# Performance work log

Hardware: AMD Instinct MI355X
Metric: run time of the kernel (lower is better)

Reference implementation:

```python
import jax, jax.numpy as jnp
import numpy as np

N = 10000
E = 160000
IN_CH = 128
HID = 128
HEADS = 4
OUT_CH = 1  # forced by nn.Linear(heads, 1) applied after conv2


def _linear_params(key, out_f, in_f):
    k1, k2 = jax.random.split(key)
    bound = 1.0 / np.sqrt(in_f)
    W = jax.random.uniform(k1, (out_f, in_f), jnp.float32, -bound, bound)
    b = jax.random.uniform(k2, (out_f,), jnp.float32, -bound, bound)
    return W, b


def setup_inputs() -> dict:
    key = jax.random.key(0)
    ks = jax.random.split(key, 12)
    x = jax.random.normal(ks[0], (N, IN_CH), jnp.float32)
    edge_index = jax.random.randint(ks[1], (2, E), 0, N, jnp.int64)

    # conv1: TransformerConv(IN_CH, HID, HEADS)
    Wq1, bq1 = _linear_params(ks[2], HEADS * HID, IN_CH)
    Wk1, bk1 = _linear_params(ks[3], HEADS * HID, IN_CH)
    Wv1, bv1 = _linear_params(ks[4], HEADS * HID, IN_CH)
    Ws1, bs1 = _linear_params(ks[5], HEADS * HID, IN_CH)  # root/skip

    # conv2: TransformerConv(HID*HEADS, OUT_CH, HEADS)
    d2 = HID * HEADS
    Wq2, bq2 = _linear_params(ks[6], HEADS * OUT_CH, d2)
    Wk2, bk2 = _linear_params(ks[7], HEADS * OUT_CH, d2)
    Wv2, bv2 = _linear_params(ks[8], HEADS * OUT_CH, d2)
    Ws2, bs2 = _linear_params(ks[9], HEADS * OUT_CH, d2)

    # final nn.Linear(HEADS, 1)
    Wl, bl = _linear_params(ks[10], 1, HEADS)

    return dict(x=x, edge_index=edge_index,
                Wq1=Wq1, bq1=bq1, Wk1=Wk1, bk1=bk1, Wv1=Wv1, bv1=bv1, Ws1=Ws1, bs1=bs1,
                Wq2=Wq2, bq2=bq2, Wk2=Wk2, bk2=bk2, Wv2=Wv2, bv2=bv2, Ws2=Ws2, bs2=bs2,
                Wl=Wl, bl=bl)


def transformer_conv(x, edge_index, Wq, bq, Wk, bk, Wv, bv, Ws, bs, heads, ch):
    # PyG TransformerConv defaults: concat=True, root_weight=True, beta=False
    n = x.shape[0]
    q = (x @ Wq.T + bq).reshape(n, heads, ch)
    k = (x @ Wk.T + bk).reshape(n, heads, ch)
    v = (x @ Wv.T + bv).reshape(n, heads, ch)

    src, dst = edge_index[0], edge_index[1]  # messages flow src -> dst
    # per-edge attention logits [E, H]
    logits = jnp.einsum('ehc,ehc->eh', q[dst], k[src]) / np.sqrt(ch).astype(np.float32)

    # segment softmax over edges grouped by destination node
    seg_max = jax.ops.segment_max(logits, dst, num_segments=n)  # [N, H]
    seg_max = jnp.where(jnp.isfinite(seg_max), seg_max, 0.0)
    ex = jnp.exp(logits - seg_max[dst])
    denom = jax.ops.segment_sum(ex, dst, num_segments=n)  # [N, H]
    alpha = ex / jnp.maximum(denom[dst], 1e-16)  # [E, H]

    # scatter-aggregate weighted values
    msgs = alpha[:, :, None] * v[src]  # [E, H, C]
    out = jax.ops.segment_sum(msgs, dst, num_segments=n)  # [N, H, C]
    out = out.reshape(n, heads * ch)
    # root/skip connection
    return out + (x @ Ws.T + bs)


def reference(x, edge_index,
              Wq1, bq1, Wk1, bk1, Wv1, bv1, Ws1, bs1,
              Wq2, bq2, Wk2, bk2, Wv2, bv2, Ws2, bs2,
              Wl, bl):
    h = transformer_conv(x, edge_index, Wq1, bq1, Wk1, bk1, Wv1, bv1, Ws1, bs1, HEADS, HID)
    h = jax.nn.relu(h)
    # dropout is identity in eval mode
    h = transformer_conv(h, edge_index, Wq2, bq2, Wk2, bk2, Wv2, bv2, Ws2, bs2, HEADS, OUT_CH)
    h = h @ Wl.T + bl  # [N, 1]
    return jnp.mean(h, axis=0, keepdims=True)  # [1, 1]
```

## Files before the change

kernel.cpp:

```cpp
#include <hip/hip_runtime.h>
#include <math.h>

#define NN 10000
#define NE 160000
#define NROWT 79
#define NGEMM (NROWT * 32)

typedef __attribute__((ext_vector_type(8))) short bf16x8;
typedef __attribute__((ext_vector_type(4))) float f32x4;
typedef __attribute__((ext_vector_type(2))) float f32x2;

#if defined(__has_builtin)
#if __has_builtin(__builtin_amdgcn_cvt_pk_fp8_f32) && __has_builtin(__builtin_amdgcn_cvt_pk_f32_fp8)
#define HW_FP8 1
#endif
#endif

__device__ inline ushort f2bf(float x) {
  uint u = __float_as_uint(x);
  return (ushort)((u + 0x7fffu + ((u >> 16) & 1u)) >> 16);
}

__device__ inline void unpack8(uint4 u, float* f) {
  f[0] = __uint_as_float(u.x << 16); f[1] = __uint_as_float(u.x & 0xffff0000u);
  f[2] = __uint_as_float(u.y << 16); f[3] = __uint_as_float(u.y & 0xffff0000u);
  f[4] = __uint_as_float(u.z << 16); f[5] = __uint_as_float(u.z & 0xffff0000u);
  f[6] = __uint_as_float(u.w << 16); f[7] = __uint_as_float(u.w & 0xffff0000u);
}

#ifndef HW_FP8
__device__ inline float fp8_dec1(uint b) {
  uint s = b >> 7, e = (b >> 3) & 15, m = b & 7;
  float v = (e == 0) ? ldexpf((float)m, -9) : ldexpf((float)(8 + m), (int)e - 10);
  return s ? -v : v;
}
__device__ inline uint fp8_enc1(float x) {
  uint s = (__float_as_uint(x) >> 31) << 7;
  float a = fabsf(x);
  if (!(a < 448.f)) return s | 0x7e;
  if (a < 9.765625e-4f) return s;
  int e; float m = frexpf(a, &e);
  int E = e - 1, q;
  if (E < -6) {
    q = (int)rintf(ldexpf(a, 9));
    if (q == 0) return s;
    if (q >= 8) return s | 8;
    return s | (uint)q;
  }
  q = (int)rintf(ldexpf(m, 4));
  if (q == 16) { q = 8; ++E; }
  if (E > 8 || (E == 8 && q == 15)) return s | 0x7e;
  return s | ((uint)(E + 7) << 3) | (uint)(q - 8);
}
#endif

__device__ inline uint pack4_fp8(float a, float b, float c, float d) {
#ifdef HW_FP8
  uint w = (uint)__builtin_amdgcn_cvt_pk_fp8_f32(a, b, 0, false);
  w = (uint)__builtin_amdgcn_cvt_pk_fp8_f32(c, d, (int)w, true);
  return w;
#else
  return fp8_enc1(a) | (fp8_enc1(b) << 8) | (fp8_enc1(c) << 16) | (fp8_enc1(d) << 24);
#endif
}

__device__ inline void dec8_fp8(uint lo, uint hi, float* f) {
#ifdef HW_FP8
  f32x2 p0 = __builtin_amdgcn_cvt_pk_f32_fp8((int)lo, false);
  f32x2 p1 = __builtin_amdgcn_cvt_pk_f32_fp8((int)lo, true);
  f32x2 p2 = __builtin_amdgcn_cvt_pk_f32_fp8((int)hi, false);
  f32x2 p3 = __builtin_amdgcn_cvt_pk_f32_fp8((int)hi, true);
  f[0] = p0.x; f[1] = p0.y; f[2] = p1.x; f[3] = p1.y;
  f[4] = p2.x; f[5] = p2.y; f[6] = p3.x; f[7] = p3.y;
#else
  f[0] = fp8_dec1(lo & 255); f[1] = fp8_dec1((lo >> 8) & 255);
  f[2] = fp8_dec1((lo >> 16) & 255); f[3] = fp8_dec1(lo >> 24);
  f[4] = fp8_dec1(hi & 255); f[5] = fp8_dec1((hi >> 8) & 255);
  f[6] = fp8_dec1((hi >> 16) & 255); f[7] = fp8_dec1(hi >> 24);
#endif
}

__device__ inline void dec16(uint4 u, float* f) {
  dec8_fp8(u.x, u.y, f);
  dec8_fp8(u.z, u.w, f + 8);
}

__global__ __launch_bounds__(1024) void zero_k(
    int* __restrict__ deg, float* __restrict__ out)
{
  int i = blockIdx.x * 1024 + threadIdx.x;
  if (i < NN) deg[i] = 0;
  if (i == 0) out[0] = 0.f;
}

__global__ __launch_bounds__(256) void prep_k(
    const float* __restrict__ x,
    const float* __restrict__ Wq1, const float* __restrict__ Wk1,
    const float* __restrict__ Wv1, const float* __restrict__ Ws1,
    ushort* __restrict__ x_bf, ushort* __restrict__ w1bf,
    const int* __restrict__ dst, int* __restrict__ deg)
{
  int i = blockIdx.x * 256 + threadIdx.x;
  if (i < NE) atomicAdd(&deg[dst[i]], 1);
  const int n4x = NN * 32;
  const int n4w = 512 * 128 / 4;
  if (i < n4x) {
    float4 v = ((const float4*)x)[i];
    ushort4 o;
    o.x = f2bf(v.x); o.y = f2bf(v.y); o.z = f2bf(v.z); o.w = f2bf(v.w);
    ((ushort4*)x_bf)[i] = o;
  } else {
    int c = i - n4x;
    if (c < 4 * n4w) {
      int seg = c >> 14, k = c & 16383;
      const float* W = (seg == 0) ? Wq1 : (seg == 1) ? Wk1
                     : (seg == 2) ? Wv1 : Ws1;
      float4 v = ((const float4*)W)[k];
      ushort4 o;
      o.x = f2bf(v.x); o.y = f2bf(v.y); o.z = f2bf(v.z); o.w = f2bf(v.w);
      ((ushort4*)(w1bf + ((size_t)seg << 16)))[k] = o;
    }
  }
}

__global__ __launch_bounds__(1024) void scan_k(
    const int* __restrict__ deg, int* __restrict__ rowptr,
    int* __restrict__ cursor)
{
  __shared__ int wsum[16];
  int tid = threadIdx.x;
  int base = tid * 10;
  int loc[10]; int s = 0;
  #pragma unroll
  for (int i = 0; i < 10; ++i) {
    int v = (base + i < NN) ? deg[base + i] : 0;
    loc[i] = s; s += v;
  }
  int mysum = s;
  #pragma unroll
  for (int d = 1; d < 64; d <<= 1) {
    int v = __shfl_up(s, d);
    if ((tid & 63) >= d) s += v;
  }
  if ((tid & 63) == 63) wsum[tid >> 6] = s;
  __syncthreads();
  int woff = 0;
  for (int w = 0; w < (tid >> 6); ++w) woff += wsum[w];
  int excl = woff + s - mysum;
  #pragma unroll
  for (int i = 0; i < 10; ++i) {
    int idx = base + i;
    if (idx < NN) { int r = excl + loc[i]; rowptr[idx] = r; cursor[idx] = r; }
  }
  if (tid == 1023) rowptr[NN] = woff + s;
}

__global__ __launch_bounds__(256) void gemm_scatter(
    const ushort* __restrict__ xbf, const ushort* __restrict__ wbf,
    const float* __restrict__ bq, const float* __restrict__ bk,
    const float* __restrict__ bv, const float* __restrict__ bs,
    unsigned char* __restrict__ q8, unsigned char* __restrict__ kv8,
    ushort* __restrict__ h1b,
    const int* __restrict__ src, const int* __restrict__ dst,
    int* __restrict__ cursor, int* __restrict__ csr_src)
{
  if (blockIdx.x >= NGEMM) {
    int e = (blockIdx.x - NGEMM) * 256 + threadIdx.x;
    if (e < NE) {
      int pos = atomicAdd(&cursor[dst[e]], 1);
      csr_src[pos] = src[e];
    }
    return;
  }
  __shared__ __align__(16) ushort Al[128 * 128];
  __shared__ __align__(16) ushort Bl[64 * 128];
  const int row0 = (blockIdx.x % NROWT) << 7;
  const int ncol0 = (blockIdx.x / NROWT) << 6;
  const int tid = threadIdx.x;

  #pragma unroll
  for (int i = 0; i < 8; ++i) {
    int slot = tid + (i << 8);
    int r = slot >> 4, c = slot & 15;
    int gr = row0 + r;
    uint4 v = make_uint4(0u, 0u, 0u, 0u);
    if (gr < NN) v = *(const uint4*)(xbf + (size_t)gr * 128 + (c << 3));
    *(uint4*)(Al + r * 128 + ((c ^ (r & 7)) << 3)) = v;
  }
  #pragma unroll
  for (int i = 0; i < 4; ++i) {
    int slot = tid + (i << 8);
    int r = slot >> 4, c = slot & 15;
    uint4 v = *(const uint4*)(wbf + (size_t)(ncol0 + r) * 128 + (c << 3));
    *(uint4*)(Bl + r * 128 + ((c ^ (r & 7)) << 3)) = v;
  }
  __syncthreads();

  const int wid = tid >> 6, lane = tid & 63;
  const int wm = wid >> 1, wn = wid & 1;
  const int lr = lane & 15, lkg = lane >> 4;
  const int seg = ncol0 >> 9;
  const int colInSeg = ncol0 & 511;
  const bool swp = (seg < 3);

  f32x4 acc[4][2];
  #pragma unroll
  for (int m = 0; m < 4; ++m)
    #pragma unroll
    for (int n = 0; n < 2; ++n) acc[m][n] = (f32x4){0.f, 0.f, 0.f, 0.f};

  #pragma unroll
  for (int ks = 0; ks < 4; ++ks) {
    int c16 = (ks << 2) + lkg;
    bf16x8 a[4], b[2];
    #pragma unroll
    for (int mf = 0; mf < 4; ++mf) {
      int r = (wm << 6) + (mf << 4) + lr;
      a[mf] = *(const bf16x8*)(Al + r * 128 + ((c16 ^ (r & 7)) << 3));
    }
    #pragma unroll
    for (int nf = 0; nf < 2; ++nf) {
      int r = (wn << 5) + (nf << 4) + lr;
      b[nf] = *(const bf16x8*)(Bl + r * 128 + ((c16 ^ (r & 7)) << 3));
    }
    if (swp) {
      #pragma unroll
      for (int mf = 0; mf < 4; ++mf)
        #pragma unroll
        for (int nf = 0; nf < 2; ++nf)
          acc[mf][nf] = __builtin_amdgcn_mfma_f32_16x16x32_bf16(
              b[nf], a[mf], acc[mf][nf], 0, 0, 0);
    } else {
      #pragma unroll
      for (int mf = 0; mf < 4; ++mf)
        #pragma unroll
        for (int nf = 0; nf < 2; ++nf)
          acc[mf][nf] = __builtin_amdgcn_mfma_f32_16x16x32_bf16(
              a[mf], b[nf], acc[mf][nf], 0, 0, 0);
    }
  }

  const float* bias = (seg == 0) ? bq : (seg == 1) ? bk : (seg == 2) ? bv : bs;
  if (swp) {
    unsigned char* out8 = (seg == 0) ? q8 : kv8;
    const int rs = (seg == 0) ? 512 : 1024;
    const int choff = (seg == 2) ? 512 : 0;
    const float scale = (seg == 0) ? 0.08838834764831845f : 1.f;
    #pragma unroll
    for (int mf = 0; mf < 4; ++mf) {
      int xrow = row0 + (wm << 6) + (mf << 4) + lr;
      if (xrow >= NN) continue;
      #pragma unroll
      for (int nf = 0; nf < 2; ++nf) {
        int ch = colInSeg + (wn << 5) + (nf << 4) + (lkg << 2);
        float4 bb = *(const float4*)(bias + ch);
        uint w = pack4_fp8((acc[mf][nf][0] + bb.x) * scale,
                           (acc[mf][nf][1] + bb.y) * scale,
                           (acc[mf][nf][2] + bb.z) * scale,
                           (acc[mf][nf][3] + bb.w) * scale);
        *(uint*)(out8 + (size_t)xrow * rs + choff + ch) = w;
      }
    }
  } else {
    #pragma unroll
    for (int mf = 0; mf < 4; ++mf) {
      #pragma unroll
      for (int nf = 0; nf < 2; ++nf) {
        int col = colInSeg + (wn << 5) + (nf << 4) + lr;
        float bb = bias[col];
        #pragma unroll
        for (int r = 0; r < 4; ++r) {
          int row = row0 + (wm << 6) + (mf << 4) + (lkg << 2) + r;
          if (row >= NN) continue;
          h1b[(size_t)row * 512 + col] = f2bf(acc[mf][nf][r] + bb);
        }
      }
    }
  }
}

#define EDGE_A(kvreg)                                                      \
  {                                                                        \
    float f[16]; dec16(kvreg, f);                                          \
    float t = qf[0]*f[0]+qf[1]*f[1]+qf[2]*f[2]+qf[3]*f[3]                  \
            + qf[4]*f[4]+qf[5]*f[5]+qf[6]*f[6]+qf[7]*f[7]                  \
            + qf[8]*f[8]+qf[9]*f[9]+qf[10]*f[10]+qf[11]*f[11]              \
            + qf[12]*f[12]+qf[13]*f[13]+qf[14]*f[14]+qf[15]*f[15];         \
    t += __shfl_xor(t, 1);                                                 \
    t += __shfl_xor(t, 2);                                                 \
    t += __shfl_xor(t, 4);                                                 \
    float exA = __expf(t);                                                 \
    float exO = __shfl_xor(exA, 32);                                       \
    if (kl) den += exA;                                                    \
    float exV = kl ? 0.f : exO;                                            \
    _Pragma("unroll")                                                      \
    for (int i = 0; i < 16; ++i) acc[i] = fmaf(exV, f[i], acc[i]);         \
  }

__global__ __launch_bounds__(512) void attn_l12(
    const unsigned char* __restrict__ q8, const unsigned char* __restrict__ kv8,
    const ushort* __restrict__ h1b, const int* __restrict__ rowptr,
    const int* __restrict__ csr_src,
    const float* __restrict__ Wq2, const float* __restrict__ bq2,
    const float* __restrict__ Wk2, const float* __restrict__ bk2,
    const float* __restrict__ Wv2, const float* __restrict__ bv2,
    const float* __restrict__ Ws2, const float* __restrict__ bs2,
    float* __restrict__ qkv2, float* __restrict__ acc2)
{
  __shared__ __align__(16) float W2l[16 * 512];
  __shared__ float h1l[4][512];
  __shared__ float partA[4][16][32];
  __shared__ float partD[4][4];
  const int tid = threadIdx.x;

  const float* Wm[4] = {Wq2, Wk2, Wv2, Ws2};
  #pragma unroll
  for (int k2 = 0; k2 < 4; ++k2) {
    int f4 = tid + (k2 << 9);
    int j = f4 >> 7, i4 = f4 & 127;
    float4 v = *(const float4*)(Wm[j >> 2] + (size_t)(j & 3) * 512 + (i4 << 2));
    *(float4*)(W2l + j * 512 + (i4 << 2)) = v;
  }

  const int wv = tid >> 6, lane = tid & 63;
  const int ns = wv >> 1, sub = wv & 1;
  const int n = blockIdx.x * 4 + ns;
  const bool kl = lane < 32;
  const int vl = lane & 31;

  float qf[16];
  if (kl) {
    uint4 qv = *(const uint4*)(q8 + (size_t)n * 512 + (lane << 4));
    dec16(qv, qf);
  } else {
    #pragma unroll
    for (int i = 0; i < 16; ++i) qf[i] = 0.f;
  }

  float acc[16] = {};
  float den = 0.f;
  const int e1 = rowptr[n + 1];
  int j = rowptr[n] + sub;
  for (; j + 2 < e1; j += 4) {
    int s0 = csr_src[j], s1 = csr_src[j + 2];
    uint4 a = *(const uint4*)(kv8 + (size_t)s0 * 1024 + (lane << 4));
    uint4 b = *(const uint4*)(kv8 + (size_t)s1 * 1024 + (lane << 4));
    EDGE_A(a)
    EDGE_A(b)
  }
  for (; j < e1; j += 2) {
    int s0 = csr_src[j];
    uint4 a = *(const uint4*)(kv8 + (size_t)s0 * 1024 + (lane << 4));
    EDGE_A(a)
  }

  if (sub) {
    if (!kl) {
      #pragma unroll
      for (int i = 0; i < 16; ++i) partA[ns][i][vl] = acc[i];
    } else if ((lane & 7) == 0) {
      partD[ns][lane >> 3] = den;
    }
  }
  __syncthreads();
  if (!sub) {
    if (!kl) {
      #pragma unroll
      for (int i = 0; i < 16; ++i) acc[i] += partA[ns][i][vl];
    } else {
      den += partD[ns][lane >> 3];
    }
    float dAll = kl ? den : 0.f;
    float dv = __shfl_xor(dAll, 32);
    if (!kl) {
      float inv = 1.f / fmaxf(dv, 1e-16f);
      int c0 = vl << 4;
      float sk[16];
      uint4 s0 = *(const uint4*)(h1b + (size_t)n * 512 + c0);
      uint4 s1 = *(const uint4*)(h1b + (size_t)n * 512 + c0 + 8);
      unpack8(s0, sk); unpack8(s1, sk + 8);
      #pragma unroll
      for (int i = 0; i < 16; ++i)
        h1l[ns][c0 + i] = fmaxf(sk[i] + acc[i] * inv, 0.f);
    }
  }
  __syncthreads();

  #pragma unroll
  for (int jj = 0; jj < 8; ++jj) {
    int j2 = (sub << 3) + jj;
    const float* wrow = W2l + j2 * 512;
    const float* hrow = h1l[ns];
    float p = 0.f;
    #pragma unroll
    for (int m = 0; m < 8; ++m)
      p = fmaf(hrow[lane + (m << 6)], wrow[lane + (m << 6)], p);
    p += __shfl_xor(p, 1);
    p += __shfl_xor(p, 2);
    p += __shfl_xor(p, 4);
    p += __shfl_xor(p, 8);
    p += __shfl_xor(p, 16);
    p += __shfl_xor(p, 32);
    if (lane == 0) {
      int sg = j2 >> 2, r = j2 & 3;
      const float* bb = (sg == 0) ? bq2 : (sg == 1) ? bk2
                      : (sg == 2) ? bv2 : bs2;
      float val = p + bb[r];
      if (sg < 3) qkv2[n * 12 + sg * 4 + r] = val;
      else        acc2[n * 4 + r] = val;
    }
  }
}

__global__ __launch_bounds__(256) void attn2_final(
    const float* __restrict__ qkv2, const int* __restrict__ rowptr,
    const int* __restrict__ csr_src, const float* __restrict__ acc2,
    const float* __restrict__ Wl, const float* __restrict__ bl,
    float* __restrict__ out)
{
  __shared__ float red[4];
  int t = blockIdx.x * 256 + threadIdx.x;
  int n = t >> 4, h = (t >> 2) & 3, part = t & 3;
  float q = qkv2[n * 12 + h];
  float den = 0.f, acc = 0.f;
  int e1 = rowptr[n + 1];
  for (int j = rowptr[n] + part; j < e1; j += 4) {
    int s = csr_src[j];
    float k = qkv2[s * 12 + 4 + h];
    float v = qkv2[s * 12 + 8 + h];
    float ex = __expf(q * k);
    den += ex; acc += ex * v;
  }
  den += __shfl_xor(den, 1); acc += __shfl_xor(acc, 1);
  den += __shfl_xor(den, 2); acc += __shfl_xor(acc, 2);
  float c = 0.f;
  if (part == 0)
    c = (acc2[n * 4 + h] + acc / fmaxf(den, 1e-16f)) * Wl[h] * (1.0f / NN);
  if (t == 0) c += bl[0];
  c += __shfl_xor(c, 4);
  c += __shfl_xor(c, 8);
  c += __shfl_xor(c, 16);
  c += __shfl_xor(c, 32);
  if ((threadIdx.x & 63) == 0) red[threadIdx.x >> 6] = c;
  __syncthreads();
  if (threadIdx.x == 0)
    unsafeAtomicAdd(out, red[0] + red[1] + red[2] + red[3]);
}

extern "C" void kernel_launch(void* const* d_in, const int* in_sizes, int n_in,
                              void* d_out, int out_size, void* d_ws, size_t ws_size,
                              hipStream_t stream)
{
  const float* x   = (const float*)d_in[0];
  const int*   ei  = (const int*)d_in[1];
  const float *Wq1 = (const float*)d_in[2],  *bq1 = (const float*)d_in[3];
  const float *Wk1 = (const float*)d_in[4],  *bk1 = (const float*)d_in[5];
  const float *Wv1 = (const float*)d_in[6],  *bv1 = (const float*)d_in[7];
  const float *Ws1 = (const float*)d_in[8],  *bs1 = (const float*)d_in[9];
  const float *Wq2 = (const float*)d_in[10], *bq2 = (const float*)d_in[11];
  const float *Wk2 = (const float*)d_in[12], *bk2 = (const float*)d_in[13];
  const float *Wv2 = (const float*)d_in[14], *bv2 = (const float*)d_in[15];
  const float *Ws2 = (const float*)d_in[16], *bs2 = (const float*)d_in[17];
  const float *Wl  = (const float*)d_in[18], *bl  = (const float*)d_in[19];
  const int* srcp = ei;
  const int* dstp = ei + NE;

  unsigned char* q8  = (unsigned char*)d_ws;
  unsigned char* kv8 = q8 + (size_t)NN * 512;
  ushort* x_bf = (ushort*)(kv8 + (size_t)NN * 1024);
  ushort* w1bf = x_bf + (size_t)NN * 128;
  ushort* h1b  = w1bf + (size_t)2048 * 128;
  float*  qkv2 = (float*)(h1b + (size_t)NN * 512);
  float*  acc2 = qkv2 + (size_t)NN * 12;
  int*   deg     = (int*)(acc2 + (size_t)NN * 4);
  int*   rowptr  = deg + NN;
  int*   cursor  = rowptr + NN + 1;
  int*   csr_src = cursor + NN;

  zero_k<<<10, 1024, 0, stream>>>(deg, (float*)d_out);
  {
    const int total = NN * 32 + 4 * (512 * 128 / 4);
    prep_k<<<(total + 255) / 256, 256, 0, stream>>>(
        x, Wq1, Wk1, Wv1, Ws1, x_bf, w1bf, dstp, deg);
  }
  scan_k<<<1, 1024, 0, stream>>>(deg, rowptr, cursor);

  gemm_scatter<<<NGEMM + (NE + 255) / 256, 256, 0, stream>>>(
      x_bf, w1bf, bq1, bk1, bv1, bs1, q8, kv8, h1b,
      srcp, dstp, cursor, csr_src);

  attn_l12<<<NN / 4, 512, 0, stream>>>(
      q8, kv8, h1b, rowptr, csr_src,
      Wq2, bq2, Wk2, bk2, Wv2, bv2, Ws2, bs2, qkv2, acc2);

  attn2_final<<<NN * 16 / 256, 256, 0, stream>>>(
      qkv2, rowptr, csr_src, acc2, Wl, bl, (float*)d_out);
}
```

Baseline: 140.2 us.

## Split fused layer-1 attention and layer-2 projection into separate kernels

The fused attention+layer-2 projection kernel is split into two. attn1 uses one wave per node with 4-edge unrolling and no cross-wave LDS reduction, and writes the ReLU'd h1 back into h1b as bf16 in place. A new gemm_l2 kernel computes the 16 layer-2 projections per node with one lane per node and the K dimension split across waves, reading the weights from global memory. This removes the per-block 32KB weight staging and the block syncs, and should raise occupancy. The cost is an extra kernel launch, a bf16 round trip of h1 through memory, and rounding of h1 to bf16.

```diff
diff --git a/kernel.cpp b/kernel.cpp
--- a/kernel.cpp
+++ b/kernel.cpp
@@ -297,34 +297,13 @@
     for (int i = 0; i < 16; ++i) acc[i] = fmaf(exV, f[i], acc[i]);         \
   }
 
-__global__ __launch_bounds__(512) void attn_l12(
+__global__ __launch_bounds__(256) void attn1(
     const unsigned char* __restrict__ q8, const unsigned char* __restrict__ kv8,
-    const ushort* __restrict__ h1b, const int* __restrict__ rowptr,
-    const int* __restrict__ csr_src,
-    const float* __restrict__ Wq2, const float* __restrict__ bq2,
-    const float* __restrict__ Wk2, const float* __restrict__ bk2,
-    const float* __restrict__ Wv2, const float* __restrict__ bv2,
-    const float* __restrict__ Ws2, const float* __restrict__ bs2,
-    float* __restrict__ qkv2, float* __restrict__ acc2)
-{
-  __shared__ __align__(16) float W2l[16 * 512];
-  __shared__ float h1l[4][512];
-  __shared__ float partA[4][16][32];
-  __shared__ float partD[4][4];
-  const int tid = threadIdx.x;
-
-  const float* Wm[4] = {Wq2, Wk2, Wv2, Ws2};
-  #pragma unroll
-  for (int k2 = 0; k2 < 4; ++k2) {
-    int f4 = tid + (k2 << 9);
-    int j = f4 >> 7, i4 = f4 & 127;
-    float4 v = *(const float4*)(Wm[j >> 2] + (size_t)(j & 3) * 512 + (i4 << 2));
-    *(float4*)(W2l + j * 512 + (i4 << 2)) = v;
-  }
-
-  const int wv = tid >> 6, lane = tid & 63;
-  const int ns = wv >> 1, sub = wv & 1;
-  const int n = blockIdx.x * 4 + ns;
+    const int* __restrict__ rowptr, const int* __restrict__ csr_src,
+    ushort* __restrict__ h1b)
+{
+  const int n = blockIdx.x * 4 + (threadIdx.x >> 6);
+  const int lane = threadIdx.x & 63;
   const bool kl = lane < 32;
   const int vl = lane & 31;
 
@@ -339,76 +318,96 @@
 
   float acc[16] = {};
   float den = 0.f;
+  int j = rowptr[n];
   const int e1 = rowptr[n + 1];
-  int j = rowptr[n] + sub;
-  for (; j + 2 < e1; j += 4) {
-    int s0 = csr_src[j], s1 = csr_src[j + 2];
-    uint4 a = *(const uint4*)(kv8 + (size_t)s0 * 1024 + (lane << 4));
-    uint4 b = *(const uint4*)(kv8 + (size_t)s1 * 1024 + (lane << 4));
-    EDGE_A(a)
-    EDGE_A(b)
-  }
-  for (; j < e1; j += 2) {
+  for (; j + 3 < e1; j += 4) {
+    int s0 = csr_src[j], s1 = csr_src[j + 1];
+    int s2 = csr_src[j + 2], s3 = csr_src[j + 3];
+    uint4 a0 = *(const uint4*)(kv8 + (size_t)s0 * 1024 + (lane << 4));
+    uint4 a1 = *(const uint4*)(kv8 + (size_t)s1 * 1024 + (lane << 4));
+    uint4 a2 = *(const uint4*)(kv8 + (size_t)s2 * 1024 + (lane << 4));
+    uint4 a3 = *(const uint4*)(kv8 + (size_t)s3 * 1024 + (lane << 4));
+    EDGE_A(a0)
+    EDGE_A(a1)
+    EDGE_A(a2)
+    EDGE_A(a3)
+  }
+  for (; j < e1; ++j) {
     int s0 = csr_src[j];
-    uint4 a = *(const uint4*)(kv8 + (size_t)s0 * 1024 + (lane << 4));
-    EDGE_A(a)
-  }
-
-  if (sub) {
-    if (!kl) {
+    uint4 a0 = *(const uint4*)(kv8 + (size_t)s0 * 1024 + (lane << 4));
+    EDGE_A(a0)
+  }
+
+  float dAll = kl ? den : 0.f;
+  float dv = __shfl_xor(dAll, 32);
+  if (!kl) {
+    float inv = 1.f / fmaxf(dv, 1e-16f);
+    int c0 = vl << 4;
+    float sk[16];
+    uint4 s0 = *(const uint4*)(h1b + (size_t)n * 512 + c0);
+    uint4 s1 = *(const uint4*)(h1b + (size_t)n * 512 + c0 + 8);
+    unpack8(s0, sk); unpack8(s1, sk + 8);
+    ushort o[16];
+    #pragma unroll
+    for (int i = 0; i < 16; ++i)
+      o[i] = f2bf(fmaxf(sk[i] + acc[i] * inv, 0.f));
+    uint4 w0, w1;
+    w0.x = (uint)o[0]  | ((uint)o[1]  << 16);
+    w0.y = (uint)o[2]  | ((uint)o[3]  << 16);
+    w0.z = (uint)o[4]  | ((uint)o[5]  << 16);
+    w0.w = (uint)o[6]  | ((uint)o[7]  << 16);
+    w1.x = (uint)o[8]  | ((uint)o[9]  << 16);
+    w1.y = (uint)o[10] | ((uint)o[11] << 16);
+    w1.z = (uint)o[12] | ((uint)o[13] << 16);
+    w1.w = (uint)o[14] | ((uint)o[15] << 16);
+    *(uint4*)(h1b + (size_t)n * 512 + c0) = w0;
+    *(uint4*)(h1b + (size_t)n * 512 + c0 + 8) = w1;
+  }
+}
+
+__global__ __launch_bounds__(256) void gemm_l2(
+    const ushort* __restrict__ h1b,
+    const float* __restrict__ Wq, const float* __restrict__ bq,
+    const float* __restrict__ Wk, const float* __restrict__ bk,
+    const float* __restrict__ Wv, const float* __restrict__ bv,
+    const float* __restrict__ Ws, const float* __restrict__ bs,
+    float* __restrict__ qkv2, float* __restrict__ acc2)
+{
+  __shared__ float red[4][64][17];
+  int n0 = blockIdx.x * 64;
+  int wid = threadIdx.x >> 6, lane = threadIdx.x & 63;
+  int n = n0 + lane;
+  const float* Wm[4] = {Wq, Wk, Wv, Ws};
+  float s[16] = {};
+  if (n < NN) {
+    const ushort* a = h1b + (size_t)n * 512 + wid * 128;
+    #pragma unroll 2
+    for (int i = 0; i < 128; i += 8) {
+      uint4 hv = *(const uint4*)(a + i);
+      float av[8]; unpack8(hv, av);
       #pragma unroll
-      for (int i = 0; i < 16; ++i) partA[ns][i][vl] = acc[i];
-    } else if ((lane & 7) == 0) {
-      partD[ns][lane >> 3] = den;
-    }
-  }
+      for (int j = 0; j < 16; ++j) {
+        const float* w = Wm[j >> 2] + (size_t)(j & 3) * 512 + wid * 128 + i;
+        s[j] += av[0]*w[0] + av[1]*w[1] + av[2]*w[2] + av[3]*w[3]
+              + av[4]*w[4] + av[5]*w[5] + av[6]*w[6] + av[7]*w[7];
+      }
+    }
+  }
+  #pragma unroll
+  for (int j = 0; j < 16; ++j) red[wid][lane][j] = s[j];
   __syncthreads();
-  if (!sub) {
-    if (!kl) {
-      #pragma unroll
-      for (int i = 0; i < 16; ++i) acc[i] += partA[ns][i][vl];
-    } else {
-      den += partD[ns][lane >> 3];
-    }
-    float dAll = kl ? den : 0.f;
-    float dv = __shfl_xor(dAll, 32);
-    if (!kl) {
-      float inv = 1.f / fmaxf(dv, 1e-16f);
-      int c0 = vl << 4;
-      float sk[16];
-      uint4 s0 = *(const uint4*)(h1b + (size_t)n * 512 + c0);
-      uint4 s1 = *(const uint4*)(h1b + (size_t)n * 512 + c0 + 8);
-      unpack8(s0, sk); unpack8(s1, sk + 8);
-      #pragma unroll
-      for (int i = 0; i < 16; ++i)
-        h1l[ns][c0 + i] = fmaxf(sk[i] + acc[i] * inv, 0.f);
-    }
-  }
-  __syncthreads();
-
-  #pragma unroll
-  for (int jj = 0; jj < 8; ++jj) {
-    int j2 = (sub << 3) + jj;
-    const float* wrow = W2l + j2 * 512;
-    const float* hrow = h1l[ns];
-    float p = 0.f;
-    #pragma unroll
-    for (int m = 0; m < 8; ++m)
-      p = fmaf(hrow[lane + (m << 6)], wrow[lane + (m << 6)], p);
-    p += __shfl_xor(p, 1);
-    p += __shfl_xor(p, 2);
-    p += __shfl_xor(p, 4);
-    p += __shfl_xor(p, 8);
-    p += __shfl_xor(p, 16);
-    p += __shfl_xor(p, 32);
-    if (lane == 0) {
-      int sg = j2 >> 2, r = j2 & 3;
-      const float* bb = (sg == 0) ? bq2 : (sg == 1) ? bk2
-                      : (sg == 2) ? bv2 : bs2;
-      float val = p + bb[r];
-      if (sg < 3) qkv2[n * 12 + sg * 4 + r] = val;
-      else        acc2[n * 4 + r] = val;
-    }
+  #pragma unroll
+  for (int q = 0; q < 4; ++q) {
+    int idx = threadIdx.x * 4 + q;
+    int ln = idx >> 4, j = idx & 15;
+    int nn2 = n0 + ln;
+    if (nn2 >= NN) continue;
+    float v = red[0][ln][j] + red[1][ln][j] + red[2][ln][j] + red[3][ln][j];
+    int sg = j >> 2, r = j & 3;
+    const float* bb = (sg == 0) ? bq : (sg == 1) ? bk : (sg == 2) ? bv : bs;
+    v += bb[r];
+    if (sg < 3) qkv2[nn2 * 12 + sg * 4 + r] = v;
+    else        acc2[nn2 * 4 + r] = v;
   }
 }
 
@@ -489,9 +488,10 @@
       x_bf, w1bf, bq1, bk1, bv1, bs1, q8, kv8, h1b,
       srcp, dstp, cursor, csr_src);
 
-  attn_l12<<<NN / 4, 512, 0, stream>>>(
-      q8, kv8, h1b, rowptr, csr_src,
-      Wq2, bq2, Wk2, bk2, Wv2, bv2, Ws2, bs2, qkv2, acc2);
+  attn1<<<NN / 4, 256, 0, stream>>>(q8, kv8, rowptr, csr_src, h1b);
+
+  gemm_l2<<<(NN + 63) / 64, 256, 0, stream>>>(
+      h1b, Wq2, bq2, Wk2, bk2, Wv2, bv2, Ws2, bs2, qkv2, acc2);
 
   attn2_final<<<NN * 16 / 256, 256, 0, stream>>>(
       qkv2, rowptr, csr_src, acc2, Wl, bl, (float*)d_out);
```

New measurement: 136.7 us. 1.03x faster.
